# Kernel optimization log

Measured on AMD Instinct MI355X. Metric: run time of the kernel, lower is better.

The kernel has to match this reference:

```python
import jax, jax.numpy as jnp
import numpy as np

NUM_UNITS = 1024
NUM_HEADS = 16


def setup_inputs() -> dict:
    key = jax.random.key(0)
    kq, kk, kv = jax.random.split(key, 3)
    B, T, U = 4, 2048, NUM_UNITS
    return {
        "querys": jax.random.normal(kq, (B, T, U), dtype=jnp.float32),
        "keys": jax.random.normal(kk, (B, T, U), dtype=jnp.float32),
        "values": jax.random.normal(kv, (B, T, U), dtype=jnp.float32),
    }


def reference(querys, keys, values):
    B, Tq, U = querys.shape
    Tk = keys.shape[1]
    H = NUM_HEADS
    D = U // H  # split_size (head dim)
    # torch.split(dim=2) + stack(dim=0) -> [H, B, T, D]
    q = querys.reshape(B, Tq, H, D).transpose(2, 0, 1, 3)
    k = keys.reshape(B, Tk, H, D).transpose(2, 0, 1, 3)
    v = values.reshape(B, Tk, H, D).transpose(2, 0, 1, 3)
    scores = jnp.einsum("hbqd,hbkd->hbqk", q, k) / jnp.sqrt(jnp.float32(D))
    probs = jax.nn.softmax(scores, axis=3)
    out = jnp.einsum("hbqk,hbkd->hbqd", probs, v)  # [H, B, Tq, D]
    # cat(split(dim=0), dim=3).squeeze(0) -> [B, Tq, H*D] with head-major concat
    return out.transpose(1, 2, 0, 3).reshape(B, Tq, H * D)
```

## Files before the change

### kernel.cpp

```cpp
#include <hip/hip_runtime.h>

#define T_SEQ 2048
#define U_DIM 1024
#define H_HEADS 16
#define D_HEAD 64
#define B_BATCH 4
#define KVBLK 64
#define QBLK 128
#define NITER (T_SEQ / KVBLK)

typedef float f32x16 __attribute__((ext_vector_type(16)));
typedef float f32x4  __attribute__((ext_vector_type(4)));
typedef __bf16 bf16x8 __attribute__((ext_vector_type(8)));
typedef unsigned int uint4v __attribute__((ext_vector_type(4)));
typedef unsigned int uint2v __attribute__((ext_vector_type(2)));
typedef unsigned short u16;

#if __has_builtin(__builtin_amdgcn_exp2f)
#define EXP2(x) __builtin_amdgcn_exp2f(x)
#else
#define EXP2(x) exp2f(x)
#endif

__device__ __forceinline__ unsigned f2bf_pack(float lo, float hi) {
    __bf16 a = (__bf16)lo, b = (__bf16)hi;
    unsigned short ua = __builtin_bit_cast(unsigned short, a);
    unsigned short ub = __builtin_bit_cast(unsigned short, b);
    return (unsigned)ua | ((unsigned)ub << 16);
}

__device__ __forceinline__ void gl2lds16(const void* g, void* l) {
    __builtin_amdgcn_global_load_lds(
        (const __attribute__((address_space(1))) void*)g,
        (__attribute__((address_space(3))) void*)l, 16, 0, 0);
}

__global__ __launch_bounds__(256) void conv_k(const float* __restrict__ K, u16* __restrict__ Kb) {
    unsigned idx = blockIdx.x * 256u + threadIdx.x;
    unsigned d8 = idx & 7, t = (idx >> 3) & 2047, h = (idx >> 14) & 15, b = idx >> 18;
    const float* src = K + (((size_t)(b * 2048 + t)) * 1024 + h * 64 + d8 * 8);
    f32x4 a = *(const f32x4*)src;
    f32x4 c = *(const f32x4*)(src + 4);
    uint4v u = { f2bf_pack(a.x, a.y), f2bf_pack(a.z, a.w),
                 f2bf_pack(c.x, c.y), f2bf_pack(c.z, c.w) };
    *(uint4v*)(Kb + (((size_t)(b * 16 + h) * 2048 + t) * 64 + d8 * 8)) = u;
}

__global__ __launch_bounds__(256) void transp_v(const float* __restrict__ V, u16* __restrict__ Vt) {
    __shared__ __align__(16) u16 tile[64][72];
    const int tid = threadIdx.x;
    const int bid = blockIdx.x;
    const int tt = bid & 31, h = (bid >> 5) & 15, b = bid >> 9;
    const int t0 = tt * 64;
    {
        const int r = tid >> 2, q = tid & 3;
        const float* src = V + (((size_t)(b * 2048 + t0 + r)) * 1024 + h * 64 + q * 16);
        f32x4 v0 = *(const f32x4*)(src);
        f32x4 v1 = *(const f32x4*)(src + 4);
        f32x4 v2 = *(const f32x4*)(src + 8);
        f32x4 v3 = *(const f32x4*)(src + 12);
#pragma unroll
        for (int j = 0; j < 4; ++j) {
            tile[q * 16 + 0  + j][r] = __builtin_bit_cast(u16, (__bf16)v0[j]);
            tile[q * 16 + 4  + j][r] = __builtin_bit_cast(u16, (__bf16)v1[j]);
            tile[q * 16 + 8  + j][r] = __builtin_bit_cast(u16, (__bf16)v2[j]);
            tile[q * 16 + 12 + j][r] = __builtin_bit_cast(u16, (__bf16)v3[j]);
        }
    }
    __syncthreads();
    {
        const int d = tid >> 2, q = tid & 3;
        u16* dst = Vt + (((size_t)(b * 16 + h) * 64 + d) * 2048 + t0 + q * 16);
        *(uint4v*)(dst)     = *(const uint4v*)&tile[d][q * 16];
        *(uint4v*)(dst + 8) = *(const uint4v*)&tile[d][q * 16 + 8];
    }
}

__global__ __launch_bounds__(256, 4) void mha_fwd4(
    const float* __restrict__ Q, const u16* __restrict__ Kb,
    const u16* __restrict__ Vt, float* __restrict__ O)
{
    const int tid  = threadIdx.x;
    const int wave = tid >> 6;
    const int lane = tid & 63;
    const int li   = lane & 31;
    const int hi   = lane >> 5;
    const int sw   = (li & 7) << 4;

    const int bid = blockIdx.x;
    const int bh  = bid & 63;
    const int qt  = bid >> 6;
    const int b   = bh >> 4;

    __shared__ __align__(16) u16 sK[2][4096];
    __shared__ __align__(16) u16 sVt[2][4096];

    const int c0 = wave * 2;
    const int r0 = lane >> 3;
    const int innerK = ((lane & 7) * 16) ^ (r0 << 4);
    const char* kbg = (const char*)Kb + (size_t)bh * 262144;
    const char* vbg = (const char*)Vt + (size_t)bh * 262144;
    const char* kp0 = kbg + c0 * 1024 + r0 * 128 + innerK;
    const char* kp1 = kbg + (c0 + 1) * 1024 + r0 * 128 + innerK;
    const char* vp0 = vbg + (size_t)(c0 * 8 + r0) * 4096 + innerK;
    const char* vp1 = vbg + (size_t)((c0 + 1) * 8 + r0) * 4096 + innerK;

#define STAGE(BUF) do {                                                   \
        char* kd = (char*)&sK[(BUF)][0] + c0 * 1024;                      \
        gl2lds16(kp0, kd); gl2lds16(kp1, kd + 1024);                      \
        char* vd = (char*)&sVt[(BUF)][0] + c0 * 1024;                     \
        gl2lds16(vp0, vd); gl2lds16(vp1, vd + 1024);                      \
        kp0 += 8192; kp1 += 8192; vp0 += 128; vp1 += 128; } while (0)

    STAGE(0);

    const float cexp = 0.18033688011112042f;
    const int qrow = qt * QBLK + wave * 32 + li;
    const float* qp = Q + ((size_t)(b * T_SEQ + qrow) * U_DIM + (bh & 15) * D_HEAD);
    bf16x8 qfrag[4];
#pragma unroll
    for (int ds = 0; ds < 4; ++ds) {
        f32x4 a = *(const f32x4*)(qp + 16 * ds + 8 * hi);
        f32x4 c = *(const f32x4*)(qp + 16 * ds + 8 * hi + 4);
        uint4v u = { f2bf_pack(a.x * cexp, a.y * cexp), f2bf_pack(a.z * cexp, a.w * cexp),
                     f2bf_pack(c.x * cexp, c.y * cexp), f2bf_pack(c.z * cexp, c.w * cexp) };
        qfrag[ds] = __builtin_bit_cast(bf16x8, u);
    }

    float l0 = 0.0f, l1 = 0.0f;
    f32x16 accO0 = {}, accO1 = {};
    int buf = 0;

    for (int it = 0; it < NITER; ++it) {
        asm volatile("s_waitcnt vmcnt(0)" ::: "memory");
        __builtin_amdgcn_s_barrier();
        asm volatile("" ::: "memory");
        if (it + 1 < NITER) { STAGE(buf ^ 1); }

        const char* kb_l = (const char*)&sK[buf][0];
        const char* vb_l = (const char*)&sVt[buf][0];

        f32x16 s0 = {}, s1 = {};
        __builtin_amdgcn_s_setprio(1);

#pragma unroll
        for (int ds = 0; ds < 4; ++ds) {
            bf16x8 kf0 = *(const bf16x8*)(kb_l + li * 128 + ((32 * ds + 16 * hi) ^ sw));
            s0 = __builtin_amdgcn_mfma_f32_32x32x16_bf16(kf0, qfrag[ds], s0, 0, 0, 0);
        }

#pragma unroll
        for (int ds = 0; ds < 4; ++ds) {
            bf16x8 kf1 = *(const bf16x8*)(kb_l + (32 + li) * 128 + ((32 * ds + 16 * hi) ^ sw));
            s1 = __builtin_amdgcn_mfma_f32_32x32x16_bf16(kf1, qfrag[ds], s1, 0, 0, 0);
            s0[4 * ds + 0] = EXP2(s0[4 * ds + 0]);
            s0[4 * ds + 1] = EXP2(s0[4 * ds + 1]);
            s0[4 * ds + 2] = EXP2(s0[4 * ds + 2]);
            s0[4 * ds + 3] = EXP2(s0[4 * ds + 3]);
        }

#pragma unroll
        for (int ks = 0; ks < 2; ++ks) {
            bf16x8 vta = *(const bf16x8*)(vb_l + li * 128 + ((32 * ks + 16 * hi) ^ sw));
            bf16x8 vtb = *(const bf16x8*)(vb_l + (32 + li) * 128 + ((32 * ks + 16 * hi) ^ sw));
            const int rb = 8 * ks;
            unsigned x1 = f2bf_pack(s0[rb + 0], s0[rb + 1]);
            unsigned x2 = f2bf_pack(s0[rb + 2], s0[rb + 3]);
            unsigned y1 = f2bf_pack(s0[rb + 4], s0[rb + 5]);
            unsigned y2 = f2bf_pack(s0[rb + 6], s0[rb + 7]);
            auto r1 = __builtin_amdgcn_permlane32_swap(x1, y1, false, false);
            auto r2 = __builtin_amdgcn_permlane32_swap(x2, y2, false, false);
            uint4v pw = { (unsigned)r1[0], (unsigned)r2[0],
                          (unsigned)r1[1], (unsigned)r2[1] };
            bf16x8 pf = __builtin_bit_cast(bf16x8, pw);
            accO0 = __builtin_amdgcn_mfma_f32_32x32x16_bf16(vta, pf, accO0, 0, 0, 0);
            accO1 = __builtin_amdgcn_mfma_f32_32x32x16_bf16(vtb, pf, accO1, 0, 0, 0);
            s1[rb + 0] = EXP2(s1[rb + 0]);
            s1[rb + 1] = EXP2(s1[rb + 1]);
            s1[rb + 2] = EXP2(s1[rb + 2]);
            s1[rb + 3] = EXP2(s1[rb + 3]);
            s1[rb + 4] = EXP2(s1[rb + 4]);
            s1[rb + 5] = EXP2(s1[rb + 5]);
            s1[rb + 6] = EXP2(s1[rb + 6]);
            s1[rb + 7] = EXP2(s1[rb + 7]);
        }

        {
            float a0 = (s0[0] + s0[1]) + (s0[2] + s0[3]);
            float a1 = (s0[4] + s0[5]) + (s0[6] + s0[7]);
            float a2 = (s0[8] + s0[9]) + (s0[10] + s0[11]);
            float a3 = (s0[12] + s0[13]) + (s0[14] + s0[15]);
            l0 += (a0 + a1) + (a2 + a3);
        }

#pragma unroll
        for (int ks = 0; ks < 2; ++ks) {
            const int kc = 2 + ks;
            bf16x8 vta = *(const bf16x8*)(vb_l + li * 128 + ((32 * kc + 16 * hi) ^ sw));
            bf16x8 vtb = *(const bf16x8*)(vb_l + (32 + li) * 128 + ((32 * kc + 16 * hi) ^ sw));
            const int rb = 8 * ks;
            unsigned x1 = f2bf_pack(s1[rb + 0], s1[rb + 1]);
            unsigned x2 = f2bf_pack(s1[rb + 2], s1[rb + 3]);
            unsigned y1 = f2bf_pack(s1[rb + 4], s1[rb + 5]);
            unsigned y2 = f2bf_pack(s1[rb + 6], s1[rb + 7]);
            auto r1 = __builtin_amdgcn_permlane32_swap(x1, y1, false, false);
            auto r2 = __builtin_amdgcn_permlane32_swap(x2, y2, false, false);
            uint4v pw = { (unsigned)r1[0], (unsigned)r2[0],
                          (unsigned)r1[1], (unsigned)r2[1] };
            bf16x8 pf = __builtin_bit_cast(bf16x8, pw);
            accO0 = __builtin_amdgcn_mfma_f32_32x32x16_bf16(vta, pf, accO0, 0, 0, 0);
            accO1 = __builtin_amdgcn_mfma_f32_32x32x16_bf16(vtb, pf, accO1, 0, 0, 0);
            float b0 = (s1[rb + 0] + s1[rb + 1]) + (s1[rb + 2] + s1[rb + 3]);
            float b1 = (s1[rb + 4] + s1[rb + 5]) + (s1[rb + 6] + s1[rb + 7]);
            l1 += b0 + b1;
        }
        __builtin_amdgcn_s_setprio(0);

        buf ^= 1;
    }
#undef STAGE

    float lsum = l0 + l1;
    float lt = lsum + __shfl_xor(lsum, 32);
    const float invl = 1.0f / lt;
    float* op = O + ((size_t)(b * T_SEQ + qrow) * U_DIM + (bh & 15) * D_HEAD);
#pragma unroll
    for (int rq = 0; rq < 4; ++rq) {
        f32x4 o0 = { accO0[4 * rq + 0] * invl, accO0[4 * rq + 1] * invl,
                     accO0[4 * rq + 2] * invl, accO0[4 * rq + 3] * invl };
        *(f32x4*)(op + 8 * rq + 4 * hi) = o0;
        f32x4 o1 = { accO1[4 * rq + 0] * invl, accO1[4 * rq + 1] * invl,
                     accO1[4 * rq + 2] * invl, accO1[4 * rq + 3] * invl };
        *(f32x4*)(op + 8 * rq + 4 * hi + 32) = o1;
    }
}

__global__ __launch_bounds__(256, 2) void mha_fwd_v1(
    const float* __restrict__ Q, const float* __restrict__ K,
    const float* __restrict__ V, float* __restrict__ O)
{
    const int tid  = threadIdx.x;
    const int wave = tid >> 6;
    const int lane = tid & 63;
    const int li   = lane & 31;
    const int hi   = lane >> 5;
    const int bid = blockIdx.x;
    const int qt  = bid & 15;
    const int bh  = bid >> 4;
    const int b   = bh >> 4;
    const int hd  = bh & 15;
    __shared__ __align__(16) u16 sK[KVBLK * D_HEAD];
    __shared__ __align__(16) u16 sV[KVBLK * D_HEAD];
    const int qrow = qt * QBLK + wave * 32 + li;
    const float* qp = Q + ((size_t)(b * T_SEQ + qrow) * U_DIM + hd * D_HEAD);
    bf16x8 qfrag[4];
#pragma unroll
    for (int ds = 0; ds < 4; ++ds) {
        f32x4 a = *(const f32x4*)(qp + 16 * ds + 8 * hi);
        f32x4 c = *(const f32x4*)(qp + 16 * ds + 8 * hi + 4);
        uint4v u = { f2bf_pack(a.x, a.y), f2bf_pack(a.z, a.w),
                     f2bf_pack(c.x, c.y), f2bf_pack(c.z, c.w) };
        qfrag[ds] = __builtin_bit_cast(bf16x8, u);
    }
    const int d4 = tid & 15;
    const int kq = tid >> 4;
    const float* kbase = K + ((size_t)(b * T_SEQ) * U_DIM + hd * D_HEAD);
    const float* vbase = V + ((size_t)(b * T_SEQ) * U_DIM + hd * D_HEAD);
    const float cexp = 0.18033688011112042f;
    float m = -INFINITY, lsum = 0.0f;
    f32x16 accO0 = {}, accO1 = {};
    for (int it = 0; it < NITER; ++it) {
        const int kv0 = it * KVBLK;
        {
            const float* kr = kbase + (size_t)(kv0 + 4 * kq) * U_DIM + 4 * d4;
            const float* vr = vbase + (size_t)(kv0 + 4 * kq) * U_DIM + 4 * d4;
            f32x4 kv[4], vv[4];
#pragma unroll
            for (int i = 0; i < 4; ++i) {
                kv[i] = *(const f32x4*)(kr + i * U_DIM);
                vv[i] = *(const f32x4*)(vr + i * U_DIM);
            }
#pragma unroll
            for (int i = 0; i < 4; ++i) {
                int row = 4 * kq + i;
                char* dst = (char*)sK + row * 128 + ((8 * d4) ^ ((row & 7) << 4));
                uint2v w = { f2bf_pack(kv[i].x, kv[i].y), f2bf_pack(kv[i].z, kv[i].w) };
                *(uint2v*)dst = w;
            }
#pragma unroll
            for (int jj = 0; jj < 4; ++jj) {
                int row = 4 * d4 + jj;
                char* dst = (char*)sV + row * 128 + ((8 * kq) << 0 ? ((8 * kq) ^ ((row & 7) << 4)) : 0);
                uint2v w = { f2bf_pack(vv[0][jj], vv[1][jj]),
                             f2bf_pack(vv[2][jj], vv[3][jj]) };
                *(uint2v*)((char*)sV + row * 128 + ((8 * kq) ^ ((row & 7) << 4))) = w;
                (void)dst;
            }
        }
        __syncthreads();
        f32x16 s0 = {}, s1 = {};
#pragma unroll
        for (int ds = 0; ds < 4; ++ds) {
            bf16x8 kf0 = *(const bf16x8*)((const char*)sK + li * 128 +
                                          ((32 * ds + 16 * hi) ^ ((li & 7) << 4)));
            bf16x8 kf1 = *(const bf16x8*)((const char*)sK + (32 + li) * 128 +
                                          ((32 * ds + 16 * hi) ^ ((li & 7) << 4)));
            s0 = __builtin_amdgcn_mfma_f32_32x32x16_bf16(kf0, qfrag[ds], s0, 0, 0, 0);
            s1 = __builtin_amdgcn_mfma_f32_32x32x16_bf16(kf1, qfrag[ds], s1, 0, 0, 0);
        }
        float tm = s0[0];
#pragma unroll
        for (int r = 1; r < 16; ++r) tm = fmaxf(tm, s0[r]);
#pragma unroll
        for (int r = 0; r < 16; ++r) tm = fmaxf(tm, s1[r]);
        tm = fmaxf(tm, __shfl_xor(tm, 32));
        if (__any(tm > m + 8.0f)) {
            float nm = fmaxf(m, tm);
            float alpha = exp2f((m - nm) * cexp);
            m = nm;
            lsum *= alpha;
#pragma unroll
            for (int r = 0; r < 16; ++r) { accO0[r] *= alpha; accO1[r] *= alpha; }
        }
        const float mc = m * cexp;
        f32x16 pv0, pv1;
        float psum = 0.0f;
#pragma unroll
        for (int r = 0; r < 16; ++r) { pv0[r] = exp2f(fmaf(s0[r], cexp, -mc)); psum += pv0[r]; }
#pragma unroll
        for (int r = 0; r < 16; ++r) { pv1[r] = exp2f(fmaf(s1[r], cexp, -mc)); psum += pv1[r]; }
        psum += __shfl_xor(psum, 32);
        lsum += psum;
        bf16x8 vt[8];
#pragma unroll
        for (int db = 0; db < 2; ++db)
#pragma unroll
            for (int ks = 0; ks < 4; ++ks)
                vt[db * 4 + ks] = *(const bf16x8*)((const char*)sV + (32 * db + li) * 128 +
                                                   ((32 * ks + 16 * hi) ^ ((li & 7) << 4)));
#define PV_STEP(ks, PV)                                                              \
        {                                                                            \
            const int rb = 8 * ((ks) & 1);                                           \
            unsigned x1 = f2bf_pack(PV[rb + 0], PV[rb + 1]);                         \
            unsigned x2 = f2bf_pack(PV[rb + 2], PV[rb + 3]);                         \
            unsigned y1 = f2bf_pack(PV[rb + 4], PV[rb + 5]);                         \
            unsigned y2 = f2bf_pack(PV[rb + 6], PV[rb + 7]);                         \
            auto r1 = __builtin_amdgcn_permlane32_swap(x1, y1, false, false);        \
            auto r2 = __builtin_amdgcn_permlane32_swap(x2, y2, false, false);        \
            uint4v pw = { (unsigned)r1[0], (unsigned)r2[0],                          \
                          (unsigned)r1[1], (unsigned)r2[1] };                        \
            bf16x8 pf = __builtin_bit_cast(bf16x8, pw);                              \
            accO0 = __builtin_amdgcn_mfma_f32_32x32x16_bf16(vt[(ks)],     pf, accO0, 0, 0, 0); \
            accO1 = __builtin_amdgcn_mfma_f32_32x32x16_bf16(vt[4 + (ks)], pf, accO1, 0, 0, 0); \
        }
        PV_STEP(0, pv0)
        PV_STEP(1, pv0)
        PV_STEP(2, pv1)
        PV_STEP(3, pv1)
#undef PV_STEP
        __syncthreads();
    }
    const float invl = 1.0f / lsum;
    float* op = O + ((size_t)(b * T_SEQ + qrow) * U_DIM + hd * D_HEAD);
#pragma unroll
    for (int rq = 0; rq < 4; ++rq) {
        f32x4 o0 = { accO0[4 * rq + 0] * invl, accO0[4 * rq + 1] * invl,
                     accO0[4 * rq + 2] * invl, accO0[4 * rq + 3] * invl };
        *(f32x4*)(op + 8 * rq + 4 * hi) = o0;
        f32x4 o1 = { accO1[4 * rq + 0] * invl, accO1[4 * rq + 1] * invl,
                     accO1[4 * rq + 2] * invl, accO1[4 * rq + 3] * invl };
        *(f32x4*)(op + 8 * rq + 4 * hi + 32) = o1;
    }
}

extern "C" void kernel_launch(void* const* d_in, const int* in_sizes, int n_in,
                              void* d_out, int out_size, void* d_ws, size_t ws_size,
                              hipStream_t stream) {
    const float* Q = (const float*)d_in[0];
    const float* K = (const float*)d_in[1];
    const float* V = (const float*)d_in[2];
    float* O = (float*)d_out;
    if (ws_size >= 33554432ull) {
        u16* Kb = (u16*)d_ws;
        u16* Vt = (u16*)((char*)d_ws + 16777216);
        conv_k<<<4096, 256, 0, stream>>>(K, Kb);
        transp_v<<<2048, 256, 0, stream>>>(V, Vt);
        mha_fwd4<<<1024, 256, 0, stream>>>(Q, Kb, Vt, O);
    } else {
        mha_fwd_v1<<<1024, 256, 0, stream>>>(Q, K, V, O);
    }
}
```

Baseline: 111.3 us.

## Pre-swizzle K/V into MFMA fragment order and load directly to registers

The conversion kernels now write K and V in the exact per-lane MFMA fragment layout. The attention kernel then reads each fragment with one coalesced 16-byte global load per lane into registers, dropping the LDS double buffer and the per-iteration barriers. The next tile's loads are issued during the current tile's compute as a register-level prefetch. This removes LDS traffic and sync, but each wave now loads K/V itself (four times the global/L2 traffic per block), register pressure rises, and launch bounds drop to 2 blocks per SM.

```diff
diff --git a/kernel.cpp b/kernel.cpp
--- a/kernel.cpp
+++ b/kernel.cpp
@@ -6,7 +6,6 @@
 #define D_HEAD 64
 #define B_BATCH 4
 #define KVBLK 64
-#define QBLK 128
 #define NITER (T_SEQ / KVBLK)
 
 typedef float f32x16 __attribute__((ext_vector_type(16)));
@@ -29,93 +28,98 @@
     return (unsigned)ua | ((unsigned)ub << 16);
 }
 
-__device__ __forceinline__ void gl2lds16(const void* g, void* l) {
-    __builtin_amdgcn_global_load_lds(
-        (const __attribute__((address_space(1))) void*)g,
-        (__attribute__((address_space(3))) void*)l, 16, 0, 0);
-}
-
-__global__ __launch_bounds__(256) void conv_k(const float* __restrict__ K, u16* __restrict__ Kb) {
-    unsigned idx = blockIdx.x * 256u + threadIdx.x;
-    unsigned d8 = idx & 7, t = (idx >> 3) & 2047, h = (idx >> 14) & 15, b = idx >> 18;
-    const float* src = K + (((size_t)(b * 2048 + t)) * 1024 + h * 64 + d8 * 8);
-    f32x4 a = *(const f32x4*)src;
-    f32x4 c = *(const f32x4*)(src + 4);
-    uint4v u = { f2bf_pack(a.x, a.y), f2bf_pack(a.z, a.w),
-                 f2bf_pack(c.x, c.y), f2bf_pack(c.z, c.w) };
-    *(uint4v*)(Kb + (((size_t)(b * 16 + h) * 2048 + t) * 64 + d8 * 8)) = u;
-}
-
-__global__ __launch_bounds__(256) void transp_v(const float* __restrict__ V, u16* __restrict__ Vt) {
+__global__ __launch_bounds__(256) void conv_kf(const float* __restrict__ K, u16* __restrict__ Kf) {
     __shared__ __align__(16) u16 tile[64][72];
     const int tid = threadIdx.x;
     const int bid = blockIdx.x;
-    const int tt = bid & 31, h = (bid >> 5) & 15, b = bid >> 9;
-    const int t0 = tt * 64;
+    const int tl = bid & 31, bh = bid >> 5;
+    const int b = bh >> 4, h = bh & 15;
     {
         const int r = tid >> 2, q = tid & 3;
-        const float* src = V + (((size_t)(b * 2048 + t0 + r)) * 1024 + h * 64 + q * 16);
+        const float* src = K + (((size_t)(b * 2048 + tl * 64 + r)) * 1024 + h * 64 + q * 16);
         f32x4 v0 = *(const f32x4*)(src);
         f32x4 v1 = *(const f32x4*)(src + 4);
         f32x4 v2 = *(const f32x4*)(src + 8);
         f32x4 v3 = *(const f32x4*)(src + 12);
-#pragma unroll
-        for (int j = 0; j < 4; ++j) {
-            tile[q * 16 + 0  + j][r] = __builtin_bit_cast(u16, (__bf16)v0[j]);
-            tile[q * 16 + 4  + j][r] = __builtin_bit_cast(u16, (__bf16)v1[j]);
-            tile[q * 16 + 8  + j][r] = __builtin_bit_cast(u16, (__bf16)v2[j]);
-            tile[q * 16 + 12 + j][r] = __builtin_bit_cast(u16, (__bf16)v3[j]);
-        }
+        uint4v w0 = { f2bf_pack(v0.x, v0.y), f2bf_pack(v0.z, v0.w),
+                      f2bf_pack(v1.x, v1.y), f2bf_pack(v1.z, v1.w) };
+        uint4v w1 = { f2bf_pack(v2.x, v2.y), f2bf_pack(v2.z, v2.w),
+                      f2bf_pack(v3.x, v3.y), f2bf_pack(v3.z, v3.w) };
+        *(uint4v*)&tile[r][q * 16]     = w0;
+        *(uint4v*)&tile[r][q * 16 + 8] = w1;
     }
     __syncthreads();
+    u16* dst = Kf + (size_t)bh * 131072 + (size_t)tl * 4096;
+#pragma unroll
+    for (int i = 0; i < 2; ++i) {
+        const int j = tid + 256 * i;
+        const int c = j >> 6, l = j & 63;
+        const int li = l & 31, hi2 = l >> 5;
+        const int half = c >> 2, ds = c & 3;
+        const int row = 32 * half + li, d0 = 16 * ds + 8 * hi2;
+        *(uint4v*)(dst + j * 8) = *(const uint4v*)&tile[row][d0];
+    }
+}
+
+__global__ __launch_bounds__(256) void conv_vf(const float* __restrict__ V, u16* __restrict__ Vf) {
+    __shared__ __align__(16) u16 tile[64][72];
+    const int tid = threadIdx.x;
+    const int bid = blockIdx.x;
+    const int tl = bid & 31, bh = bid >> 5;
+    const int b = bh >> 4, h = bh & 15;
     {
-        const int d = tid >> 2, q = tid & 3;
-        u16* dst = Vt + (((size_t)(b * 16 + h) * 64 + d) * 2048 + t0 + q * 16);
-        *(uint4v*)(dst)     = *(const uint4v*)&tile[d][q * 16];
-        *(uint4v*)(dst + 8) = *(const uint4v*)&tile[d][q * 16 + 8];
-    }
-}
-
-__global__ __launch_bounds__(256, 4) void mha_fwd4(
-    const float* __restrict__ Q, const u16* __restrict__ Kb,
-    const u16* __restrict__ Vt, float* __restrict__ O)
+        const int r = tid >> 2, q = tid & 3;
+        const float* src = V + (((size_t)(b * 2048 + tl * 64 + r)) * 1024 + h * 64 + q * 16);
+        f32x4 v0 = *(const f32x4*)(src);
+        f32x4 v1 = *(const f32x4*)(src + 4);
+        f32x4 v2 = *(const f32x4*)(src + 8);
+        f32x4 v3 = *(const f32x4*)(src + 12);
+        uint4v w0 = { f2bf_pack(v0.x, v0.y), f2bf_pack(v0.z, v0.w),
+                      f2bf_pack(v1.x, v1.y), f2bf_pack(v1.z, v1.w) };
+        uint4v w1 = { f2bf_pack(v2.x, v2.y), f2bf_pack(v2.z, v2.w),
+                      f2bf_pack(v3.x, v3.y), f2bf_pack(v3.z, v3.w) };
+        *(uint4v*)&tile[r][q * 16]     = w0;
+        *(uint4v*)&tile[r][q * 16 + 8] = w1;
+    }
+    __syncthreads();
+    u16* dst = Vf + (size_t)bh * 131072 + (size_t)tl * 4096;
+#pragma unroll
+    for (int i = 0; i < 2; ++i) {
+        const int j = tid + 256 * i;
+        const int c = j >> 6, l = j & 63;
+        const int li = l & 31, hi2 = l >> 5;
+        const int ks = c >> 1, db = c & 1;
+        const int key0 = 16 * ks + 8 * hi2, d = 32 * db + li;
+        unsigned w0 = (unsigned)tile[key0 + 0][d] | ((unsigned)tile[key0 + 1][d] << 16);
+        unsigned w1 = (unsigned)tile[key0 + 2][d] | ((unsigned)tile[key0 + 3][d] << 16);
+        unsigned w2 = (unsigned)tile[key0 + 4][d] | ((unsigned)tile[key0 + 5][d] << 16);
+        unsigned w3 = (unsigned)tile[key0 + 6][d] | ((unsigned)tile[key0 + 7][d] << 16);
+        uint4v w = { w0, w1, w2, w3 };
+        *(uint4v*)(dst + j * 8) = w;
+    }
+}
+
+__global__ __launch_bounds__(256, 2) void mha_fwd8(
+    const float* __restrict__ Q, const u16* __restrict__ Kf,
+    const u16* __restrict__ Vf, float* __restrict__ O)
 {
     const int tid  = threadIdx.x;
     const int wave = tid >> 6;
     const int lane = tid & 63;
     const int li   = lane & 31;
     const int hi   = lane >> 5;
-    const int sw   = (li & 7) << 4;
 
     const int bid = blockIdx.x;
     const int bh  = bid & 63;
     const int qt  = bid >> 6;
     const int b   = bh >> 4;
 
-    __shared__ __align__(16) u16 sK[2][4096];
-    __shared__ __align__(16) u16 sVt[2][4096];
-
-    const int c0 = wave * 2;
-    const int r0 = lane >> 3;
-    const int innerK = ((lane & 7) * 16) ^ (r0 << 4);
-    const char* kbg = (const char*)Kb + (size_t)bh * 262144;
-    const char* vbg = (const char*)Vt + (size_t)bh * 262144;
-    const char* kp0 = kbg + c0 * 1024 + r0 * 128 + innerK;
-    const char* kp1 = kbg + (c0 + 1) * 1024 + r0 * 128 + innerK;
-    const char* vp0 = vbg + (size_t)(c0 * 8 + r0) * 4096 + innerK;
-    const char* vp1 = vbg + (size_t)((c0 + 1) * 8 + r0) * 4096 + innerK;
-
-#define STAGE(BUF) do {                                                   \
-        char* kd = (char*)&sK[(BUF)][0] + c0 * 1024;                      \
-        gl2lds16(kp0, kd); gl2lds16(kp1, kd + 1024);                      \
-        char* vd = (char*)&sVt[(BUF)][0] + c0 * 1024;                     \
-        gl2lds16(vp0, vd); gl2lds16(vp1, vd + 1024);                      \
-        kp0 += 8192; kp1 += 8192; vp0 += 128; vp1 += 128; } while (0)
-
-    STAGE(0);
+    const u16* kfb = Kf + (size_t)bh * 131072;
+    const u16* vfb = Vf + (size_t)bh * 131072;
+    const int loff = lane * 8;
 
     const float cexp = 0.18033688011112042f;
-    const int qrow = qt * QBLK + wave * 32 + li;
+    const int qrow = qt * 128 + wave * 32 + li;
     const float* qp = Q + ((size_t)(b * T_SEQ + qrow) * U_DIM + (bh & 15) * D_HEAD);
     bf16x8 qfrag[4];
 #pragma unroll
@@ -127,32 +131,30 @@
         qfrag[ds] = __builtin_bit_cast(bf16x8, u);
     }
 
+    bf16x8 kc[8], vc[8];
+#pragma unroll
+    for (int c = 0; c < 8; ++c) kc[c] = *(const bf16x8*)(kfb + c * 512 + loff);
+#pragma unroll
+    for (int c = 0; c < 8; ++c) vc[c] = *(const bf16x8*)(vfb + c * 512 + loff);
+
     float l0 = 0.0f, l1 = 0.0f;
     f32x16 accO0 = {}, accO1 = {};
-    int buf = 0;
-
+
+#pragma unroll 1
     for (int it = 0; it < NITER; ++it) {
-        asm volatile("s_waitcnt vmcnt(0)" ::: "memory");
-        __builtin_amdgcn_s_barrier();
-        asm volatile("" ::: "memory");
-        if (it + 1 < NITER) { STAGE(buf ^ 1); }
-
-        const char* kb_l = (const char*)&sK[buf][0];
-        const char* vb_l = (const char*)&sVt[buf][0];
+        const u16* kn = kfb + (size_t)(((it + 1) & 31) * 4096);
+        const u16* vn = vfb + (size_t)(((it + 1) & 31) * 4096);
 
         f32x16 s0 = {}, s1 = {};
         __builtin_amdgcn_s_setprio(1);
 
 #pragma unroll
+        for (int ds = 0; ds < 4; ++ds)
+            s0 = __builtin_amdgcn_mfma_f32_32x32x16_bf16(kc[ds], qfrag[ds], s0, 0, 0, 0);
+
+#pragma unroll
         for (int ds = 0; ds < 4; ++ds) {
-            bf16x8 kf0 = *(const bf16x8*)(kb_l + li * 128 + ((32 * ds + 16 * hi) ^ sw));
-            s0 = __builtin_amdgcn_mfma_f32_32x32x16_bf16(kf0, qfrag[ds], s0, 0, 0, 0);
-        }
-
-#pragma unroll
-        for (int ds = 0; ds < 4; ++ds) {
-            bf16x8 kf1 = *(const bf16x8*)(kb_l + (32 + li) * 128 + ((32 * ds + 16 * hi) ^ sw));
-            s1 = __builtin_amdgcn_mfma_f32_32x32x16_bf16(kf1, qfrag[ds], s1, 0, 0, 0);
+            s1 = __builtin_amdgcn_mfma_f32_32x32x16_bf16(kc[4 + ds], qfrag[ds], s1, 0, 0, 0);
             s0[4 * ds + 0] = EXP2(s0[4 * ds + 0]);
             s0[4 * ds + 1] = EXP2(s0[4 * ds + 1]);
             s0[4 * ds + 2] = EXP2(s0[4 * ds + 2]);
@@ -160,9 +162,10 @@
         }
 
 #pragma unroll
+        for (int c = 0; c < 8; ++c) kc[c] = *(const bf16x8*)(kn + c * 512 + loff);
+
+#pragma unroll
         for (int ks = 0; ks < 2; ++ks) {
-            bf16x8 vta = *(const bf16x8*)(vb_l + li * 128 + ((32 * ks + 16 * hi) ^ sw));
-            bf16x8 vtb = *(const bf16x8*)(vb_l + (32 + li) * 128 + ((32 * ks + 16 * hi) ^ sw));
             const int rb = 8 * ks;
             unsigned x1 = f2bf_pack(s0[rb + 0], s0[rb + 1]);
             unsigned x2 = f2bf_pack(s0[rb + 2], s0[rb + 3]);
@@ -173,8 +176,8 @@
             uint4v pw = { (unsigned)r1[0], (unsigned)r2[0],
                           (unsigned)r1[1], (unsigned)r2[1] };
             bf16x8 pf = __builtin_bit_cast(bf16x8, pw);
-            accO0 = __builtin_amdgcn_mfma_f32_32x32x16_bf16(vta, pf, accO0, 0, 0, 0);
-            accO1 = __builtin_amdgcn_mfma_f32_32x32x16_bf16(vtb, pf, accO1, 0, 0, 0);
+            accO0 = __builtin_amdgcn_mfma_f32_32x32x16_bf16(vc[2 * ks], pf, accO0, 0, 0, 0);
+            accO1 = __builtin_amdgcn_mfma_f32_32x32x16_bf16(vc[2 * ks + 1], pf, accO1, 0, 0, 0);
             s1[rb + 0] = EXP2(s1[rb + 0]);
             s1[rb + 1] = EXP2(s1[rb + 1]);
             s1[rb + 2] = EXP2(s1[rb + 2]);
@@ -195,9 +198,7 @@
 
 #pragma unroll
         for (int ks = 0; ks < 2; ++ks) {
-            const int kc = 2 + ks;
-            bf16x8 vta = *(const bf16x8*)(vb_l + li * 128 + ((32 * kc + 16 * hi) ^ sw));
-            bf16x8 vtb = *(const bf16x8*)(vb_l + (32 + li) * 128 + ((32 * kc + 16 * hi) ^ sw));
+            const int kc2 = 2 + ks;
             const int rb = 8 * ks;
             unsigned x1 = f2bf_pack(s1[rb + 0], s1[rb + 1]);
             unsigned x2 = f2bf_pack(s1[rb + 2], s1[rb + 3]);
@@ -208,17 +209,18 @@
             uint4v pw = { (unsigned)r1[0], (unsigned)r2[0],
                           (unsigned)r1[1], (unsigned)r2[1] };
             bf16x8 pf = __builtin_bit_cast(bf16x8, pw);
-            accO0 = __builtin_amdgcn_mfma_f32_32x32x16_bf16(vta, pf, accO0, 0, 0, 0);
-            accO1 = __builtin_amdgcn_mfma_f32_32x32x16_bf16(vtb, pf, accO1, 0, 0, 0);
+            accO0 = __builtin_amdgcn_mfma_f32_32x32x16_bf16(vc[2 * kc2], pf, accO0, 0, 0, 0);
+            accO1 = __builtin_amdgcn_mfma_f32_32x32x16_bf16(vc[2 * kc2 + 1], pf, accO1, 0, 0, 0);
             float b0 = (s1[rb + 0] + s1[rb + 1]) + (s1[rb + 2] + s1[rb + 3]);
             float b1 = (s1[rb + 4] + s1[rb + 5]) + (s1[rb + 6] + s1[rb + 7]);
             l1 += b0 + b1;
         }
+
+#pragma unroll
+        for (int c = 0; c < 8; ++c) vc[c] = *(const bf16x8*)(vn + c * 512 + loff);
+
         __builtin_amdgcn_s_setprio(0);
-
-        buf ^= 1;
-    }
-#undef STAGE
+    }
 
     float lsum = l0 + l1;
     float lt = lsum + __shfl_xor(lsum, 32);
@@ -251,7 +253,7 @@
     const int hd  = bh & 15;
     __shared__ __align__(16) u16 sK[KVBLK * D_HEAD];
     __shared__ __align__(16) u16 sV[KVBLK * D_HEAD];
-    const int qrow = qt * QBLK + wave * 32 + li;
+    const int qrow = qt * 128 + wave * 32 + li;
     const float* qp = Q + ((size_t)(b * T_SEQ + qrow) * U_DIM + hd * D_HEAD);
     bf16x8 qfrag[4];
 #pragma unroll
@@ -290,11 +292,9 @@
 #pragma unroll
             for (int jj = 0; jj < 4; ++jj) {
                 int row = 4 * d4 + jj;
-                char* dst = (char*)sV + row * 128 + ((8 * kq) << 0 ? ((8 * kq) ^ ((row & 7) << 4)) : 0);
                 uint2v w = { f2bf_pack(vv[0][jj], vv[1][jj]),
                              f2bf_pack(vv[2][jj], vv[3][jj]) };
                 *(uint2v*)((char*)sV + row * 128 + ((8 * kq) ^ ((row & 7) << 4))) = w;
-                (void)dst;
             }
         }
         __syncthreads();
@@ -381,11 +381,11 @@
     const float* V = (const float*)d_in[2];
     float* O = (float*)d_out;
     if (ws_size >= 33554432ull) {
-        u16* Kb = (u16*)d_ws;
-        u16* Vt = (u16*)((char*)d_ws + 16777216);
-        conv_k<<<4096, 256, 0, stream>>>(K, Kb);
-        transp_v<<<2048, 256, 0, stream>>>(V, Vt);
-        mha_fwd4<<<1024, 256, 0, stream>>>(Q, Kb, Vt, O);
+        u16* Kf = (u16*)d_ws;
+        u16* Vf = (u16*)((char*)d_ws + 16777216);
+        conv_kf<<<2048, 256, 0, stream>>>(K, Kf);
+        conv_vf<<<2048, 256, 0, stream>>>(V, Vf);
+        mha_fwd8<<<1024, 256, 0, stream>>>(Q, Kf, Vf, O);
     } else {
         mha_fwd_v1<<<1024, 256, 0, stream>>>(Q, K, V, O);
     }
```

Measured after the change: 117.9 us. +6.0%, slower.
